# Optimization experiments

Measured on AMD Instinct MI355X. Metric: run time of the kernel, lower is better.

## Reference

```python
import jax, jax.numpy as jnp
import numpy as np

B, T, C = 4, 2048, 1024


def setup_inputs() -> dict:
    key = jax.random.key(0)
    ks = jax.random.split(key, 7)
    s = 1.0 / np.sqrt(C)
    return {
        "x": jax.random.normal(ks[0], (B, T, C), dtype=jnp.float32),
        "Wq": jax.random.normal(ks[1], (C, C), dtype=jnp.float32) * s,
        "bq": jnp.zeros((C,), dtype=jnp.float32),
        "Wk": jax.random.normal(ks[2], (C, C), dtype=jnp.float32) * s,
        "bk": jnp.zeros((C,), dtype=jnp.float32),
        "Wv": jax.random.normal(ks[3], (C, C), dtype=jnp.float32) * s,
        "bv": jnp.zeros((C,), dtype=jnp.float32),
    }


def reference(x, Wq, bq, Wk, bk, Wv, bv):
    # q/k/v projections (torch Linear: x @ W^T + b; here W stored as [C_in, C_out])
    q = x @ Wq + bq  # (B, T, C)
    k = x @ Wk + bk
    v = x @ Wv + bv
    scale = 1.0 / jnp.sqrt(jnp.asarray(C, dtype=x.dtype))
    att = jnp.einsum("btc,bsc->bts", q, k) * scale  # (B, T, T)
    # causal mask: additive -inf above the diagonal
    causal = jnp.tril(jnp.ones((T, T), dtype=bool))
    att = jnp.where(causal, att, jnp.asarray(-jnp.inf, dtype=att.dtype))
    att = jax.nn.softmax(att, axis=-1)
    # dropout is identity in eval/reference mode
    out = jnp.einsum("bts,bsc->btc", att, v)  # (B, T, C)
    return out
```

## Files before the change

### kernel.cpp

```cpp
#include <hip/hip_runtime.h>

#define B_ 4
#define T_ 2048
#define C_ 1024

typedef unsigned short u16;
typedef unsigned int u32;
typedef short sh8 __attribute__((ext_vector_type(8)));
typedef float f32x4 __attribute__((ext_vector_type(4)));

__device__ __forceinline__ float bf2f(u16 u) {
    union { float f; u32 i; } c; c.i = ((u32)u) << 16; return c.f;
}
__device__ __forceinline__ u16 f2bf(float f) {
    union { float f; u32 i; } c; c.f = f;
    return (u16)((c.i + 0x7FFFu + ((c.i >> 16) & 1u)) >> 16);
}

__device__ __forceinline__ void gload_lds16(const void* g, void* l) {
    __builtin_amdgcn_global_load_lds(
        (const __attribute__((address_space(1))) u32*)g,
        (__attribute__((address_space(3))) u32*)l, 16, 0, 0);
}

__device__ __forceinline__ void wait_vm8()   { asm volatile("s_waitcnt vmcnt(8)" ::: "memory"); }
__device__ __forceinline__ void wait_vm0()   { asm volatile("s_waitcnt vmcnt(0)" ::: "memory"); }
__device__ __forceinline__ void barrier_raw(){ asm volatile("s_barrier" ::: "memory"); }

template<bool RS>
__device__ __forceinline__ void mm_core(
    const u16* __restrict__ A, const u16* __restrict__ B,
    int ldA, int ldB, int nk64,
    u16* lds, f32x4 (&acc)[4][4], f32x4* rsacc, int tid)
{
    const int w  = tid >> 6, l = tid & 63;
    const int fr = l & 15,  fq = l >> 4;
    const int wm = (w & 1) << 6, wn = (w >> 1) << 6;
    const int rl = l >> 3;
    const int pc = l & 7;
    const int cg = pc ^ rl;

    sh8 ones;
    if (RS) {
#pragma unroll
        for (int e = 0; e < 8; ++e) ones[e] = (short)0x3F80;
    }

    auto issue = [&](int kt) {
        const int ko = kt << 6;
        u16* dA = lds + ((kt & 1) << 14);
        u16* dB = dA + 8192;
#pragma unroll
        for (int t = 0; t < 4; ++t) {
            const int r0 = w * 32 + t * 8;
            const int r  = r0 + rl;
            gload_lds16(A + (size_t)r * ldA + ko + cg * 8, dA + ((size_t)r0 * 8 + l) * 8);
            gload_lds16(B + (size_t)r * ldB + ko + cg * 8, dB + ((size_t)r0 * 8 + l) * 8);
        }
    };

    issue(0);
    issue(1);

    for (int kt = 0; kt < nk64; ++kt) {
        if (kt + 1 < nk64) wait_vm8(); else wait_vm0();
        barrier_raw();
        u16* bufA = lds + ((kt & 1) << 14);
        u16* bufB = bufA + 8192;
#pragma unroll
        for (int kk = 0; kk < 2; ++kk) {
            sh8 af[4], bf[4];
            const int g = kk * 4 + fq;
#pragma unroll
            for (int i = 0; i < 4; ++i) {
                const int m = wm + i * 16 + fr;
                af[i] = *(const sh8*)(bufA + ((size_t)m * 8 + (g ^ (m & 7))) * 8);
                const int n = wn + i * 16 + fr;
                bf[i] = *(const sh8*)(bufB + ((size_t)n * 8 + (g ^ (n & 7))) * 8);
            }
#pragma unroll
            for (int i = 0; i < 4; ++i) {
#pragma unroll
                for (int j = 0; j < 4; ++j)
                    acc[i][j] = __builtin_amdgcn_mfma_f32_16x16x32_bf16(af[i], bf[j], acc[i][j], 0, 0, 0);
                if (RS)
                    rsacc[i] = __builtin_amdgcn_mfma_f32_16x16x32_bf16(af[i], ones, rsacc[i], 0, 0, 0);
            }
        }
        barrier_raw();
        if (kt + 2 < nk64) issue(kt + 2);
    }
}

__global__ __launch_bounds__(256) void cvt_all(
    const float* __restrict__ x,
    const float* __restrict__ Wq, const float* __restrict__ Wk, const float* __restrict__ Wv,
    u16* __restrict__ xb, u16* __restrict__ wt)
{
    __shared__ float tile[64][68];
    const int bid = blockIdx.x;
    if (bid < 8192) {
        size_t i = ((size_t)bid * 256 + threadIdx.x) * 4;
        float4 f = *(const float4*)(x + i);
        ushort4 o;
        o.x = f2bf(f.x); o.y = f2bf(f.y); o.z = f2bf(f.z); o.w = f2bf(f.w);
        *(ushort4*)(xb + i) = o;
        return;
    }
    const int r = bid - 8192;
    const int z = r >> 8;
    const int rr = r & 255;
    const int n0 = (rr & 15) * 64, k0 = (rr >> 4) * 64;
    const float* W = z == 0 ? Wq : (z == 1 ? Wk : Wv);
    u16* out = wt + (size_t)z * C_ * C_;
    const int tx = threadIdx.x & 15, ty = threadIdx.x >> 4;
#pragma unroll
    for (int rr2 = 0; rr2 < 4; ++rr2) {
        int row = ty + rr2 * 16;
        *(float4*)&tile[row][tx * 4] = *(const float4*)(W + (size_t)(k0 + row) * C_ + n0 + tx * 4);
    }
    __syncthreads();
#pragma unroll
    for (int rr2 = 0; rr2 < 4; ++rr2) {
        int n = ty + rr2 * 16;
        ushort4 o;
        o.x = f2bf(tile[tx * 4 + 0][n]);
        o.y = f2bf(tile[tx * 4 + 1][n]);
        o.z = f2bf(tile[tx * 4 + 2][n]);
        o.w = f2bf(tile[tx * 4 + 3][n]);
        *(ushort4*)(out + (size_t)(n0 + n) * C_ + k0 + tx * 4) = o;
    }
}

__global__ __launch_bounds__(256, 2) void qkv_f(
    const u16* __restrict__ xb, const u16* __restrict__ wt,
    const float* __restrict__ bq, const float* __restrict__ bk, const float* __restrict__ bv,
    u16* __restrict__ qo, u16* __restrict__ ko, u16* __restrict__ vto)
{
    __shared__ __align__(16) u16 smem[32768];
    const int x = blockIdx.x;
    const int z = x >> 9;
    const int inner = x & 511;
    const int mt = ((inner & 7) << 3) + (inner >> 6);
    const int nt = (inner >> 3) & 7;
    const int m0 = mt << 7, n0 = nt << 7;
    const u16* W = wt + (size_t)z * C_ * C_;
    const float* bias = z == 0 ? bq : (z == 1 ? bk : bv);
    const int tid = threadIdx.x;
    f32x4 acc[4][4];
#pragma unroll
    for (int i = 0; i < 4; ++i)
#pragma unroll
        for (int j = 0; j < 4; ++j) acc[i][j] = 0.0f;

    mm_core<false>(xb + (size_t)m0 * C_, W + (size_t)n0 * C_, C_, C_, C_ / 64, smem, acc, nullptr, tid);

    const int w = tid >> 6, l = tid & 63, fr = l & 15, fq = l >> 4;
    const int wm = (w & 1) << 6, wn = (w >> 1) << 6;
    if (z < 2) {
#pragma unroll
        for (int i = 0; i < 4; ++i)
#pragma unroll
            for (int j = 0; j < 4; ++j) {
                const int ln = wn + j * 16 + fr;
                const float bb = bias[n0 + ln];
#pragma unroll
                for (int r = 0; r < 4; ++r) {
                    const int lm = wm + i * 16 + fq * 4 + r;
                    smem[lm * 136 + ln] = f2bf(acc[i][j][r] + bb);
                }
            }
        __syncthreads();
        u16* out = z == 0 ? qo : ko;
        const int rr = tid >> 4, cc = tid & 15;
#pragma unroll
        for (int p = 0; p < 8; ++p) {
            const int row = p * 16 + rr;
            uint4 val = *(const uint4*)&smem[row * 136 + cc * 8];
            *(uint4*)(out + (size_t)(m0 + row) * C_ + n0 + cc * 8) = val;
        }
    } else {
#pragma unroll
        for (int i = 0; i < 4; ++i)
#pragma unroll
            for (int j = 0; j < 4; ++j) {
                const int ln = wn + j * 16 + fr;
                const float bb = bias[n0 + ln];
#pragma unroll
                for (int r = 0; r < 4; ++r) {
                    const int lm = wm + i * 16 + fq * 4 + r;
                    smem[lm * 129 + ln] = f2bf(acc[i][j][r] + bb);
                }
            }
        __syncthreads();
        const int b = m0 >> 11;
        const int t0 = m0 & 2047;
        u16* vt = vto + (size_t)b * C_ * T_;
#pragma unroll
        for (int pass = 0; pass < 8; ++pass) {
            const int ln = (tid >> 4) + pass * 16;
            const int c  = tid & 15;
            u16 tmp[8];
#pragma unroll
            for (int e = 0; e < 8; ++e) tmp[e] = smem[(c * 8 + e) * 129 + ln];
            *(uint4*)(vt + (size_t)(n0 + ln) * T_ + t0 + c * 8) = *(uint4*)tmp;
        }
    }
}

__device__ __constant__ size_t att_off[4] = {
    0, (size_t)1 << 22, (size_t)1 << 25, ((size_t)1 << 25) + ((size_t)1 << 22)
};

__global__ __launch_bounds__(256, 2) void scores_mfma(
    const u16* __restrict__ qb, const u16* __restrict__ kb, u16* __restrict__ wsbase)
{
    int t = blockIdx.x;
    int by = (int)((sqrtf(8.f * t + 1.f) - 1.f) * 0.5f);
    while ((by + 1) * (by + 2) / 2 <= t) ++by;
    while (by * (by + 1) / 2 > t) --by;
    const int bx = t - by * (by + 1) / 2;
    const int b = blockIdx.z;
    const int s0 = bx * 128, m0 = by * 128;
    __shared__ __align__(16) u16 smem[32768];
    const u16* Q = qb + (size_t)b * T_ * C_ + (size_t)m0 * C_;
    const u16* K = kb + (size_t)b * T_ * C_ + (size_t)s0 * C_;
    const int tid = threadIdx.x;
    f32x4 acc[4][4];
#pragma unroll
    for (int i = 0; i < 4; ++i)
#pragma unroll
        for (int j = 0; j < 4; ++j) acc[i][j] = 0.0f;

    mm_core<false>(Q, K, C_, C_, C_ / 64, smem, acc, nullptr, tid);

    const int w = tid >> 6, l = tid & 63, fr = l & 15, fq = l >> 4;
    const int wm = (w & 1) << 6, wn = (w >> 1) << 6;
#pragma unroll
    for (int i = 0; i < 4; ++i)
#pragma unroll
        for (int r = 0; r < 4; ++r) {
            const int lm = wm + i * 16 + fq * 4 + r;
            const int m = m0 + lm;
#pragma unroll
            for (int j = 0; j < 4; ++j) {
                const int ls = wn + j * 16 + fr;
                const int s = s0 + ls;
                float e = (s <= m) ? __expf(acc[i][j][r] * 0.03125f) : 0.f;
                smem[lm * 136 + ls] = f2bf(e);
            }
        }
    __syncthreads();
    u16* att = wsbase + att_off[b] + (size_t)m0 * T_ + s0;
    const int rr = tid >> 4, cc = tid & 15;
#pragma unroll
    for (int p = 0; p < 8; ++p) {
        const int row = p * 16 + rr;
        uint4 val = *(const uint4*)&smem[row * 136 + cc * 8];
        *(uint4*)(att + (size_t)row * T_ + cc * 8) = val;
    }
}

__global__ __launch_bounds__(256, 2) void pv_mfma(
    const u16* __restrict__ wsbase, const u16* __restrict__ vt,
    float* __restrict__ outp)
{
    const int b = blockIdx.z;
    const int n0 = blockIdx.x * 128;
    const int by = (blockIdx.z < 2) ? (15 - blockIdx.y) : blockIdx.y;
    const int m0 = by * 128;
    __shared__ __align__(16) u16 smem[32768];
    const u16* A  = wsbase + att_off[b] + (size_t)m0 * T_;
    const u16* Bp = vt + (size_t)b * C_ * T_ + (size_t)n0 * T_;
    const int tid = threadIdx.x;
    f32x4 acc[4][4], rs[4];
#pragma unroll
    for (int i = 0; i < 4; ++i) {
        rs[i] = 0.0f;
#pragma unroll
        for (int j = 0; j < 4; ++j) acc[i][j] = 0.0f;
    }

    mm_core<true>(A, Bp, T_, T_, (m0 + 128) >> 6, smem, acc, rs, tid);

    const int w = tid >> 6, l = tid & 63, fr = l & 15, fq = l >> 4;
    const int wm = (w & 1) << 6, wn = (w >> 1) << 6;
    float* fb = (float*)smem;
#pragma unroll
    for (int p = 0; p < 2; ++p) {
        if ((w & 1) == p) {
#pragma unroll
            for (int i = 0; i < 4; ++i)
#pragma unroll
                for (int r = 0; r < 4; ++r) {
                    const int rr2 = i * 16 + fq * 4 + r;
                    const float inv = 1.0f / rs[i][r];
#pragma unroll
                    for (int j = 0; j < 4; ++j)
                        fb[rr2 * 132 + wn + j * 16 + fr] = acc[i][j][r] * inv;
                }
        }
        __syncthreads();
        const int rr = tid >> 5, cc = (tid & 31) * 4;
#pragma unroll
        for (int k2 = 0; k2 < 8; ++k2) {
            const int row = k2 * 8 + rr;
            float4 val = *(const float4*)&fb[row * 132 + cc];
            *(float4*)(outp + ((size_t)b * T_ + m0 + p * 64 + row) * C_ + n0 + cc) = val;
        }
        __syncthreads();
    }
}

extern "C" void kernel_launch(void* const* d_in, const int* in_sizes, int n_in,
                              void* d_out, int out_size, void* d_ws, size_t ws_size,
                              hipStream_t stream) {
    const float* x  = (const float*)d_in[0];
    const float* Wq = (const float*)d_in[1];
    const float* bq = (const float*)d_in[2];
    const float* Wk = (const float*)d_in[3];
    const float* bk = (const float*)d_in[4];
    const float* Wv = (const float*)d_in[5];
    const float* bv = (const float*)d_in[6];
    float* out = (float*)d_out;

    char* ws = (char*)d_ws;
    u16* xb   = (u16*)ws;
    u16* q    = (u16*)(ws + (16ull << 20));
    u16* k    = (u16*)(ws + (32ull << 20));
    u16* vt   = (u16*)(ws + (48ull << 20));
    u16* wt   = (u16*)(ws + (64ull << 20));
    u16* attb = (u16*)ws;

    cvt_all <<<8960, 256, 0, stream>>>(x, Wq, Wk, Wv, xb, wt);
    qkv_f   <<<1536, 256, 0, stream>>>(xb, wt, bq, bk, bv, q, k, vt);
    scores_mfma<<<dim3(136, 1, 4), 256, 0, stream>>>(q, k, attb);
    pv_mfma    <<<dim3(8, 16, 4), 256, 0, stream>>>(attb, vt, out);
}
```

Before: 223.4 us.

## Compute softmax row sums in scores kernel, split QKV launch, remap score blocks

Moves the softmax denominator out of the PV GEMM. Each scores block sums its bf16 exp tile per row and atomically adds the result into a global rowsum buffer, which is zeroed by extra blocks in the convert kernel. This removes the ones-vector MFMA that PV ran at every k step. The single QKV launch is split into three launches, one per projection, and the scores grid is flattened with an interleaved batch/tile mapping, which may improve cache locality. The costs are the atomics, the extra launches, and float atomic ordering that is no longer deterministic.

```diff
diff --git a/kernel.cpp b/kernel.cpp
--- a/kernel.cpp
+++ b/kernel.cpp
@@ -8,6 +8,8 @@
 typedef unsigned int u32;
 typedef short sh8 __attribute__((ext_vector_type(8)));
 typedef float f32x4 __attribute__((ext_vector_type(4)));
+
+__device__ float rowsum_g[4 * 2048];
 
 __device__ __forceinline__ float bf2f(u16 u) {
     union { float f; u32 i; } c; c.i = ((u32)u) << 16; return c.f;
@@ -99,6 +101,13 @@
 {
     __shared__ float tile[64][68];
     const int bid = blockIdx.x;
+    if (bid >= 8960) {
+        float* p = rowsum_g + (size_t)(bid - 8960) * 4096 + threadIdx.x * 16;
+        const float4 z4 = {0.f, 0.f, 0.f, 0.f};
+#pragma unroll
+        for (int e = 0; e < 4; ++e) ((float4*)p)[e] = z4;
+        return;
+    }
     if (bid < 8192) {
         size_t i = ((size_t)bid * 256 + threadIdx.x) * 4;
         float4 f = *(const float4*)(x + i);
@@ -132,20 +141,16 @@
     }
 }
 
-__global__ __launch_bounds__(256, 2) void qkv_f(
-    const u16* __restrict__ xb, const u16* __restrict__ wt,
-    const float* __restrict__ bq, const float* __restrict__ bk, const float* __restrict__ bv,
-    u16* __restrict__ qo, u16* __restrict__ ko, u16* __restrict__ vto)
+__global__ __launch_bounds__(256, 2) void qkv_z(
+    const u16* __restrict__ xb, const u16* __restrict__ W,
+    const float* __restrict__ bias,
+    u16* __restrict__ out, int isv)
 {
     __shared__ __align__(16) u16 smem[32768];
     const int x = blockIdx.x;
-    const int z = x >> 9;
-    const int inner = x & 511;
-    const int mt = ((inner & 7) << 3) + (inner >> 6);
-    const int nt = (inner >> 3) & 7;
+    const int mt = ((x & 7) << 3) + (x >> 6);
+    const int nt = (x >> 3) & 7;
     const int m0 = mt << 7, n0 = nt << 7;
-    const u16* W = wt + (size_t)z * C_ * C_;
-    const float* bias = z == 0 ? bq : (z == 1 ? bk : bv);
     const int tid = threadIdx.x;
     f32x4 acc[4][4];
 #pragma unroll
@@ -157,7 +162,7 @@
 
     const int w = tid >> 6, l = tid & 63, fr = l & 15, fq = l >> 4;
     const int wm = (w & 1) << 6, wn = (w >> 1) << 6;
-    if (z < 2) {
+    if (!isv) {
 #pragma unroll
         for (int i = 0; i < 4; ++i)
 #pragma unroll
@@ -171,7 +176,6 @@
                 }
             }
         __syncthreads();
-        u16* out = z == 0 ? qo : ko;
         const int rr = tid >> 4, cc = tid & 15;
 #pragma unroll
         for (int p = 0; p < 8; ++p) {
@@ -195,7 +199,7 @@
         __syncthreads();
         const int b = m0 >> 11;
         const int t0 = m0 & 2047;
-        u16* vt = vto + (size_t)b * C_ * T_;
+        u16* vt = out + (size_t)b * C_ * T_;
 #pragma unroll
         for (int pass = 0; pass < 8; ++pass) {
             const int ln = (tid >> 4) + pass * 16;
@@ -215,12 +219,14 @@
 __global__ __launch_bounds__(256, 2) void scores_mfma(
     const u16* __restrict__ qb, const u16* __restrict__ kb, u16* __restrict__ wsbase)
 {
-    int t = blockIdx.x;
+    const int id = blockIdx.x;
+    const int s_ = (id & 7) * 68 + (id >> 3);
+    const int b  = s_ / 136;
+    int t = s_ - b * 136;
     int by = (int)((sqrtf(8.f * t + 1.f) - 1.f) * 0.5f);
     while ((by + 1) * (by + 2) / 2 <= t) ++by;
     while (by * (by + 1) / 2 > t) --by;
     const int bx = t - by * (by + 1) / 2;
-    const int b = blockIdx.z;
     const int s0 = bx * 128, m0 = by * 128;
     __shared__ __align__(16) u16 smem[32768];
     const u16* Q = qb + (size_t)b * T_ * C_ + (size_t)m0 * C_;
@@ -258,6 +264,15 @@
         const int row = p * 16 + rr;
         uint4 val = *(const uint4*)&smem[row * 136 + cc * 8];
         *(uint4*)(att + (size_t)row * T_ + cc * 8) = val;
+    }
+    {
+        const int r2 = tid >> 1, half = tid & 1;
+        const u16* rowp = &smem[r2 * 136 + half * 64];
+        float ssum = 0.f;
+#pragma unroll
+        for (int e = 0; e < 64; ++e) ssum += bf2f(rowp[e]);
+        ssum += __shfl_xor(ssum, 1);
+        if (!half) atomicAdd(&rowsum_g[b * 2048 + m0 + r2], ssum);
     }
 }
 
@@ -273,15 +288,13 @@
     const u16* A  = wsbase + att_off[b] + (size_t)m0 * T_;
     const u16* Bp = vt + (size_t)b * C_ * T_ + (size_t)n0 * T_;
     const int tid = threadIdx.x;
-    f32x4 acc[4][4], rs[4];
-#pragma unroll
-    for (int i = 0; i < 4; ++i) {
-        rs[i] = 0.0f;
+    f32x4 acc[4][4];
+#pragma unroll
+    for (int i = 0; i < 4; ++i)
 #pragma unroll
         for (int j = 0; j < 4; ++j) acc[i][j] = 0.0f;
-    }
-
-    mm_core<true>(A, Bp, T_, T_, (m0 + 128) >> 6, smem, acc, rs, tid);
+
+    mm_core<false>(A, Bp, T_, T_, (m0 + 128) >> 6, smem, acc, nullptr, tid);
 
     const int w = tid >> 6, l = tid & 63, fr = l & 15, fq = l >> 4;
     const int wm = (w & 1) << 6, wn = (w >> 1) << 6;
@@ -294,7 +307,7 @@
 #pragma unroll
                 for (int r = 0; r < 4; ++r) {
                     const int rr2 = i * 16 + fq * 4 + r;
-                    const float inv = 1.0f / rs[i][r];
+                    const float inv = 1.0f / rowsum_g[b * 2048 + m0 + wm + rr2];
 #pragma unroll
                     for (int j = 0; j < 4; ++j)
                         fb[rr2 * 132 + wn + j * 16 + fr] = acc[i][j][r] * inv;
@@ -332,8 +345,10 @@
     u16* wt   = (u16*)(ws + (64ull << 20));
     u16* attb = (u16*)ws;
 
-    cvt_all <<<8960, 256, 0, stream>>>(x, Wq, Wk, Wv, xb, wt);
-    qkv_f   <<<1536, 256, 0, stream>>>(xb, wt, bq, bk, bv, q, k, vt);
-    scores_mfma<<<dim3(136, 1, 4), 256, 0, stream>>>(q, k, attb);
+    cvt_all <<<8962, 256, 0, stream>>>(x, Wq, Wk, Wv, xb, wt);
+    qkv_z   <<<512, 256, 0, stream>>>(xb, wt,                   bq, q,  0);
+    qkv_z   <<<512, 256, 0, stream>>>(xb, wt + (size_t)C_*C_,   bk, k,  0);
+    qkv_z   <<<512, 256, 0, stream>>>(xb, wt + (size_t)2*C_*C_, bv, vt, 1);
+    scores_mfma<<<544, 256, 0, stream>>>(q, k, attb);
     pv_mfma    <<<dim3(8, 16, 4), 256, 0, stream>>>(attb, vt, out);
 }
```

After: 224.6 us. No clear change (+0.5%).
